# Kernel optimization log

Hardware: AMD Instinct MI355X
Metric: run time of the kernel (lower is better)

The kernel has to match this reference:

```python
import jax, jax.numpy as jnp
from jax import lax
import numpy as np

TEMPERATURE = 0.8
TOP_P = 0.9
NEG_INF = -jnp.inf


def setup_inputs() -> dict:
    key = jax.random.key(0)
    k1, k2 = jax.random.split(key)
    B, V = 128, 128000
    logits = jax.random.normal(k1, (B, V), dtype=jnp.float32) * 4.0
    u = jax.random.uniform(k2, (B, 1), dtype=jnp.float32)  # replaces torch.rand in sample_multinomial
    return {"logits": logits, "u": u, "top_k": 50}


def _filtered_probs(logits, top_k):
    # temperature scaling
    x = logits / TEMPERATURE
    # ---- top-k filter: keep only the k largest per row (mask rest to -inf) ----
    kth = lax.top_k(x, top_k)[0][..., -1:]            # [B, 1] k-th largest value
    x = jnp.where(x < kth, NEG_INF, x)
    # ---- top-p (nucleus) filter ----
    sort_idx = jnp.argsort(-x, axis=-1)               # descending order, [B, V]
    sorted_x = jnp.take_along_axis(x, sort_idx, axis=-1)
    probs_sorted = jax.nn.softmax(sorted_x, axis=-1)  # -inf entries -> 0
    cdf = jnp.cumsum(probs_sorted, axis=-1)
    # remove tokens where cdf (shifted right by one, first kept) exceeds p
    remove_sorted = jnp.concatenate(
        [jnp.zeros_like(cdf[..., :1], dtype=bool), (cdf > TOP_P)[..., :-1]], axis=-1
    )
    inv = jnp.argsort(sort_idx, axis=-1)              # inverse permutation
    remove = jnp.take_along_axis(remove_sorted, inv, axis=-1)
    x = jnp.where(remove, NEG_INF, x)
    # final probabilities
    return jax.nn.softmax(x.astype(jnp.float32), axis=-1)


def reference(logits, u, top_k):
    probs = _filtered_probs(logits, top_k)            # [B, V]
    # inverse-CDF multinomial sample (matches sample_multinomial)
    csum = jnp.cumsum(probs, axis=-1)
    next_ids = jnp.sum(csum <= u, axis=-1, keepdims=True).astype(jnp.int32)  # [B, 1]
    return next_ids
```

## Files before the change

kernel.cpp:

```cpp
#include <hip/hip_runtime.h>
#include <math.h>


#define SLICES   16
#define SEGCAP   64
#define MSORT    1024

__device__ __forceinline__ unsigned fkey(float y) {
    unsigned b = __float_as_uint(y);
    return (b & 0x80000000u) ? ~b : (b | 0x80000000u);
}

__device__ __forceinline__ float block_sum(float v, int tid, float* wpart) {
#pragma unroll
    for (int off = 32; off > 0; off >>= 1) v += __shfl_down(v, off, 64);
    if ((tid & 63) == 0) wpart[tid >> 6] = v;
    __syncthreads();
    if (tid < 64) {
        float s = (tid < 16) ? wpart[tid] : 0.0f;
#pragma unroll
        for (int off = 8; off > 0; off >>= 1) s += __shfl_down(s, off, 64);
        if (tid == 0) wpart[0] = s;
    }
    __syncthreads();
    float s = wpart[0];
    __syncthreads();
    return s;
}

__device__ __forceinline__ void incl_scan(float* arr, int n, int tid, float* wpart) {
    float v = (tid < n) ? arr[tid] : 0.0f;
#pragma unroll
    for (int off = 1; off < 64; off <<= 1) {
        float o = __shfl_up(v, off, 64);
        if ((tid & 63) >= off) v += o;
    }
    if ((tid & 63) == 63) wpart[tid >> 6] = v;
    __syncthreads();
    if (tid < 64) {
        float w = (tid < 16) ? wpart[tid] : 0.0f;
#pragma unroll
        for (int off = 1; off < 16; off <<= 1) {
            float o = __shfl_up(w, off, 64);
            if (tid >= off) w += o;
        }
        if (tid < 16) wpart[tid] = w;
    }
    __syncthreads();
    const int wv = tid >> 6;
    const float base = (wv > 0) ? wpart[wv - 1] : 0.0f;
    if (tid < n) arr[tid] = v + base;
    __syncthreads();
}

__device__ __forceinline__ float wsum(float v) {
#pragma unroll
    for (int off = 32; off > 0; off >>= 1) v += __shfl_xor(v, off, 64);
    return v;
}
__device__ __forceinline__ float wscan(float v, int lane) {
#pragma unroll
    for (int off = 1; off < 64; off <<= 1) {
        float o = __shfl_up(v, off, 64);
        if (lane >= off) v += o;
    }
    return v;
}

__global__ __launch_bounds__(256)
void scan_kernel(const float* __restrict__ logits, int V,
                 int* __restrict__ scnt,
                 float* __restrict__ cy, int* __restrict__ ci)
{
    constexpr float YTH = 11.2f;
    __shared__ float lcy[SEGCAP];
    __shared__ int   lci[SEGCAP];
    __shared__ int   lcnt;

    const int tid = threadIdx.x;
    const int row = blockIdx.x / SLICES;
    const int sl  = blockIdx.x % SLICES;
    if (tid == 0) lcnt = 0;
    __syncthreads();

    const float* rowp = logits + (size_t)row * (size_t)V;
    const float4* rp4 = (const float4*)rowp;
    const int n4   = V >> 2;
    const int base = sl * 256 + tid;

#define PUSH4(vv, i4)                                                            \
    {                                                                            \
        float _m = fmaxf(fmaxf((vv).x, (vv).y), fmaxf((vv).z, (vv).w));          \
        if (_m >= YTH) {                                                         \
            if ((vv).x >= YTH) { int _p = atomicAdd(&lcnt, 1);                   \
                if (_p < SEGCAP) { lcy[_p] = (vv).x; lci[_p] = (i4) * 4;     } } \
            if ((vv).y >= YTH) { int _p = atomicAdd(&lcnt, 1);                   \
                if (_p < SEGCAP) { lcy[_p] = (vv).y; lci[_p] = (i4) * 4 + 1; } } \
            if ((vv).z >= YTH) { int _p = atomicAdd(&lcnt, 1);                   \
                if (_p < SEGCAP) { lcy[_p] = (vv).z; lci[_p] = (i4) * 4 + 2; } } \
            if ((vv).w >= YTH) { int _p = atomicAdd(&lcnt, 1);                   \
                if (_p < SEGCAP) { lcy[_p] = (vv).w; lci[_p] = (i4) * 4 + 3; } } \
        }                                                                        \
    }

    if (sl * 256 + 255 + 7 * 4096 < n4) {
        float4 a0 = rp4[base];
        float4 a1 = rp4[base + 4096];
        float4 a2 = rp4[base + 8192];
        float4 a3 = rp4[base + 12288];
        float4 a4 = rp4[base + 16384];
        float4 a5 = rp4[base + 20480];
        float4 a6 = rp4[base + 24576];
        float4 a7 = rp4[base + 28672];
        PUSH4(a0, base);
        PUSH4(a1, base + 4096);
        PUSH4(a2, base + 8192);
        PUSH4(a3, base + 12288);
        PUSH4(a4, base + 16384);
        PUSH4(a5, base + 20480);
        PUSH4(a6, base + 24576);
        PUSH4(a7, base + 28672);
    } else {
        const int nc = n4 - 1;
        int i0 = base,          c0 = min(i0, nc);
        int i1 = base + 4096,   c1 = min(i1, nc);
        int i2 = base + 8192,   c2 = min(i2, nc);
        int i3 = base + 12288,  c3 = min(i3, nc);
        int i4_ = base + 16384, c4 = min(i4_, nc);
        int i5 = base + 20480,  c5 = min(i5, nc);
        int i6 = base + 24576,  c6 = min(i6, nc);
        int i7 = base + 28672,  c7 = min(i7, nc);
        float4 a0 = rp4[c0];
        float4 a1 = rp4[c1];
        float4 a2 = rp4[c2];
        float4 a3 = rp4[c3];
        float4 a4 = rp4[c4];
        float4 a5 = rp4[c5];
        float4 a6 = rp4[c6];
        float4 a7 = rp4[c7];
        if (i0 < n4) PUSH4(a0, i0);
        if (i1 < n4) PUSH4(a1, i1);
        if (i2 < n4) PUSH4(a2, i2);
        if (i3 < n4) PUSH4(a3, i3);
        if (i4_ < n4) PUSH4(a4, i4_);
        if (i5 < n4) PUSH4(a5, i5);
        if (i6 < n4) PUSH4(a6, i6);
        if (i7 < n4) PUSH4(a7, i7);
    }
    for (int i = SLICES * 256 * 8 + sl * 256 + tid; i < n4; i += SLICES * 256) {
        float4 a = rp4[i];
        PUSH4(a, i);
    }
    if (sl == SLICES - 1) {
        for (int i = (n4 << 2) + tid; i < V; i += 256) {
            float y = rowp[i];
            if (y >= YTH) {
                int p = atomicAdd(&lcnt, 1);
                if (p < SEGCAP) { lcy[p] = y; lci[p] = i; }
            }
        }
    }
#undef PUSH4
    __syncthreads();

    const int cnt = lcnt;
    float* cyr = cy + ((size_t)row * SLICES + sl) * SEGCAP;
    int*   cir = ci + ((size_t)row * SLICES + sl) * SEGCAP;
    for (int p = tid; p < min(cnt, SEGCAP); p += 256) {
        cyr[p] = lcy[p];
        cir[p] = lci[p];
    }
    if (tid == 0) scnt[row * SLICES + sl] = cnt;
}

__global__ __launch_bounds__(1024)
void select_kernel(const float* __restrict__ logits,
                   const float* __restrict__ uvec,
                   const int* __restrict__ topk_p,
                   const int* __restrict__ scnt,
                   const float* __restrict__ cy, const int* __restrict__ ci,
                   int* __restrict__ out, int V)
{
    constexpr float TEMP = 0.8f;
    constexpr float TOPP = 0.9f;
    constexpr float XTH2 = 16.0f;

    __shared__ float gv[MSORT];
    __shared__ int   gi[MSORT];
    __shared__ float cv[MSORT];
    __shared__ int   cidx[MSORT];
    __shared__ float sq[MSORT];
    __shared__ float wpart[16];
    __shared__ float kth_sh;
    __shared__ int   segoff[SLICES + 1];
    __shared__ int   bad_sh, hi_cnt, cpos, scount, cnt_sh, M_sh, tie_cnt, L_cnt, ans_sh;
    __shared__ int   Kp_sh, fast_sh;

    const int tid  = threadIdx.x;
    const int lane = tid & 63;
    const int row  = blockIdx.x;
    const int nth  = blockDim.x;
    const int k_in = *topk_p;

    const float* rowp = logits + (size_t)row * (size_t)V;

    if (tid == 0) { hi_cnt = 0; cpos = 0; scount = 0;
                    tie_cnt = 0; L_cnt = 0; ans_sh = V; }
    if (tid < 64) {
        int c = (tid < SLICES) ? scnt[row * SLICES + tid] : 0;
        int bad = (tid < SLICES) && (c > SEGCAP);
        int acc = min(c, SEGCAP);
#pragma unroll
        for (int off = 1; off < SLICES; off <<= 1) {
            int o = __shfl_up(acc, off, 64);
            if (tid >= off) acc += o;
        }
        if (tid < SLICES) segoff[tid + 1] = acc;
        if (tid == 0) segoff[0] = 0;
        unsigned long long bm = __ballot(bad);
        if (tid == 0) bad_sh = (bm != 0ULL);
    }
    __syncthreads();

    const int M_all = segoff[SLICES];
    int M;
    if (!bad_sh && M_all >= k_in && M_all <= MSORT) {
        {
            const int s = tid >> 6;
            const int off = segoff[s];
            const int c   = segoff[s + 1] - off;
            if (lane < c) {
                const size_t base = ((size_t)row * SLICES + s) * SEGCAP + lane;
                gv[off + lane] = cy[base] / TEMP;
                gi[off + lane] = ci[base];
            }
        }
        __syncthreads();
        {
            bool pred = (tid < M_all) && (gv[tid] >= XTH2);
            unsigned long long bm = __ballot(pred);
            if (lane == 0 && bm) atomicAdd(&hi_cnt, (int)__popcll(bm));
        }
        __syncthreads();
        const float thr = (hi_cnt >= k_in) ? XTH2 : -1e38f;
        {
            bool pred = (tid < M_all) && (gv[tid] >= thr);
            unsigned long long bm = __ballot(pred);
            if (bm) {
                int fl = (int)__ffsll(bm) - 1;
                int bs = 0;
                if (pred && lane == fl) bs = atomicAdd(&cpos, (int)__popcll(bm));
                bs = __shfl(bs, fl, 64);
                if (pred) {
                    int p = bs + (int)__popcll(bm & ((1ULL << lane) - 1ULL));
                    cv[p] = gv[tid]; cidx[p] = gi[tid];
                }
            }
        }
        __syncthreads();
        M = cpos;
    } else {
        unsigned lo = 0;
        for (int bit = 31; bit >= 0; --bit) {
            unsigned t = lo | (1u << bit);
            int local = 0;
            for (int i = tid; i < V; i += nth) local += (fkey(rowp[i]) >= t);
            if (tid == 0) cnt_sh = 0;
            __syncthreads();
            atomicAdd(&cnt_sh, local);
            __syncthreads();
            if (cnt_sh >= k_in) lo = t;
            __syncthreads();
        }
        for (int i = tid; i < V; i += nth) {
            float y = rowp[i];
            if (fkey(y) >= lo) {
                int p = atomicAdd(&scount, 1);
                if (p < MSORT) { cv[p] = y / TEMP; cidx[p] = i; }
            }
        }
        __syncthreads();
        M = min(scount, MSORT);
    }
    if (tid == 0) M_sh = M;
    __syncthreads();
    M = M_sh;

    const int Mpad = (M + 3) & ~3;
    for (int t = M + tid; t < Mpad; t += nth) { cv[t] = -1e38f; cidx[t] = 0x7fffffff; }
    __syncthreads();

    for (int t = tid; t < M; t += nth) {
        const float v = cv[t]; const int ix = cidx[t];
        int r = 0;
        for (int j = 0; j < Mpad; j += 4) {
            float v0 = cv[j],     v1 = cv[j + 1];
            float v2 = cv[j + 2], v3 = cv[j + 3];
            int   i0 = cidx[j],     i1 = cidx[j + 1];
            int   i2 = cidx[j + 2], i3 = cidx[j + 3];
            r += (v0 > v || (v0 == v && i0 < ix));
            r += (v1 > v || (v1 == v && i1 < ix));
            r += (v2 > v || (v2 == v && i2 < ix));
            r += (v3 > v || (v3 == v && i3 < ix));
        }
        gv[r] = v; gi[r] = ix;
    }
    __syncthreads();

    if (tid < 64) {
        int kk = (M > 0) ? min(max(k_in, 1), M) : 0;
        float kth = (M > 0) ? gv[kk - 1] : 0.0f;
        int j0 = min(kk + lane, MSORT - 1);
        int j1 = min(kk + 64 + lane, MSORT - 1);
        bool t0 = (M > 0) && (kk + lane < M)      && (gv[j0] == kth);
        bool t1 = (M > 0) && (kk + 64 + lane < M) && (gv[j1] == kth);
        int cnt = (int)__popcll(__ballot(t0)) + (int)__popcll(__ballot(t1));
        if (lane == 0) {
            int Kp = kk + cnt;
            Kp_sh = Kp;
            fast_sh = (M > 0) && (Kp <= 128);
        }
    }
    __syncthreads();

    if (fast_sh) {
        if (tid < 64) {
            const int Kp = Kp_sh;
            const int e0 = lane, e1 = lane + 64;
            const float mm = gv[0];
            float se0 = (e0 < Kp) ? expf(gv[e0] - mm) : 0.0f;
            float se1 = (e1 < Kp) ? expf(gv[e1] - mm) : 0.0f;

            const float sum1 = wsum(se0 + se1);
            float q0 = se0 / sum1, q1 = se1 / sum1;

            float s0 = wscan(q0, lane);
            float T0 = __shfl(s0, 63, 64);
            float s1 = wscan(q1, lane) + T0;

            float prev0 = __shfl_up(s0, 1, 64);
            float prev1 = __shfl_up(s1, 1, 64);
            if (lane == 0) prev1 = T0;
            bool c0 = (e0 >= 1) && (e0 < Kp) && (prev0 <= TOPP);
            bool c1 = (e1 < Kp) && (prev1 <= TOPP);
            const int L = 1 + (int)__popcll(__ballot(c0)) + (int)__popcll(__ballot(c1));

            const float sum2 = wsum(((e0 < L) ? se0 : 0.0f) + ((e1 < L) ? se1 : 0.0f));
            float p0 = se0 / sum2, p1 = se1 / sum2;
            int i0 = (e0 < L) ? gi[e0] : 0x7fffffff;
            int i1 = (e1 < L) ? gi[e1] : 0x7fffffff;

            const int Lpad = (L + 3) & ~3;
            if (lane < Lpad - L) gi[L + lane] = 0x7fffffff;
            __builtin_amdgcn_wave_barrier();

            int r0 = 0, r1 = 0;
            for (int j = 0; j < Lpad; j += 4) {
                int g0 = gi[j], g1 = gi[j + 1], g2 = gi[j + 2], g3 = gi[j + 3];
                r0 += (g0 < i0) + (g1 < i0) + (g2 < i0) + (g3 < i0);
                r1 += (g0 < i1) + (g1 < i1) + (g2 < i1) + (g3 < i1);
            }
            if (e0 < L) { sq[r0] = p0; cidx[r0] = i0; }
            if (e1 < L) { sq[r1] = p1; cidx[r1] = i1; }
            __builtin_amdgcn_wave_barrier();

            float g0v = (e0 < L) ? sq[e0] : 0.0f;
            float g1v = (e1 < L) ? sq[e1] : 0.0f;
            int   vi0 = (e0 < L) ? cidx[e0] : 0;
            int   vi1 = (e1 < L) ? cidx[e1] : 0;
            float C0 = wscan(g0v, lane);
            float TT = __shfl(C0, 63, 64);
            float C1 = wscan(g1v, lane) + TT;
            float pc0 = __shfl_up(C0, 1, 64);
            float pc1 = __shfl_up(C1, 1, 64);
            if (lane == 0) pc1 = TT;
            const float uu = uvec[row];
            bool f0 = (e0 < L) && (C0 > uu) && (e0 == 0 || pc0 <= uu);
            bool f1 = (e1 < L) && (C1 > uu) && (pc1 <= uu);
            int ans = V;
            if (f0) ans = vi0;
            if (f1) ans = vi1;
#pragma unroll
            for (int off = 32; off > 0; off >>= 1)
                ans = min(ans, __shfl_xor(ans, off, 64));
            if (lane == 0) out[row] = ans;
        }
        return;
    }

    const int kk = (M > 0) ? min(max(k_in, 1), M) : 0;
    const float mm = (M > 0) ? gv[0] : 0.0f;
    if (tid < M) cv[tid] = expf(gv[tid] - mm);
    if (tid == 0 && M > 0) kth_sh = gv[kk - 1];
    __syncthreads();

    {
        bool f = (M > 0) && (tid >= kk) && (tid < M) && (gv[tid] == kth_sh);
        unsigned long long bm = __ballot(f);
        if (lane == 0 && bm) atomicAdd(&tie_cnt, (int)__popcll(bm));
    }
    __syncthreads();
    const int Kp = kk + tie_cnt;

    const float sum1 = block_sum((tid < Kp) ? cv[tid] : 0.0f, tid, wpart);

    if (tid < Kp) sq[tid] = cv[tid] / sum1;
    incl_scan(sq, Kp, tid, wpart);
    {
        bool f = (tid >= 1) && (tid < Kp) && (sq[tid - 1] <= TOPP);
        unsigned long long bm = __ballot(f);
        if (lane == 0 && bm) atomicAdd(&L_cnt, (int)__popcll(bm));
    }
    __syncthreads();
    const int L = (M > 0) ? (1 + L_cnt) : 0;

    const float sum2 = block_sum((tid < L) ? cv[tid] : 0.0f, tid, wpart);

    if (tid < L) {
        const int ix = gi[tid];
        int r = 0;
        for (int j = 0; j < L; ++j) r += (gi[j] < ix);
        sq[r] = cv[tid] / sum2;
        cidx[r] = ix;
    }
    __syncthreads();

    incl_scan(sq, L, tid, wpart);
    {
        const float uu = uvec[row];
        bool f = (tid < L) && (sq[tid] > uu) && (tid == 0 || sq[tid - 1] <= uu);
        if (f) ans_sh = cidx[tid];
    }
    __syncthreads();
    if (tid == 0) out[row] = ans_sh;
}

extern "C" void kernel_launch(void* const* d_in, const int* in_sizes, int n_in,
                              void* d_out, int out_size, void* d_ws, size_t ws_size,
                              hipStream_t stream) {
    const float* logits = (const float*)d_in[0];
    const float* u      = (const float*)d_in[1];
    const int*   topk   = (const int*)d_in[2];
    int*         out    = (int*)d_out;

    const int B = out_size;
    const int V = in_sizes[0] / B;

    const size_t n_scnt = (size_t)B * SLICES;
    const size_t n_seg  = (size_t)B * SLICES * SEGCAP;
    int*   scnt = (int*)d_ws;
    float* cy   = (float*)((char*)d_ws + n_scnt * 4);
    int*   ci   = (int*)((char*)d_ws + n_scnt * 4 + n_seg * 4);

    scan_kernel<<<B * SLICES, 256, 0, stream>>>(logits, V, scnt, cy, ci);
    select_kernel<<<B, 1024, 0, stream>>>(logits, u, topk, scnt, cy, ci, out, V);
}
```

Measured before the change: 101.3 us.

## Fuse scan and select kernels using a last-block-done atomic counter per row

Merges the two-kernel pipeline into one launch: each of the 16 slice blocks per row writes its candidates to global memory, then bumps a per-row atomic counter, and the last block to finish performs the selection with 256 threads instead of a separate 1024-thread block. This removes the second kernel launch and the dependency gap between kernels, at the cost of a hipMemsetAsync to reset counters and less parallelism in the selection phase. The slow fallback path is now serialized on a single thread, and the radix-select fallback runs with a quarter of the threads.

```diff
diff --git a/kernel.cpp b/kernel.cpp
--- a/kernel.cpp
+++ b/kernel.cpp
@@ -5,52 +5,11 @@
 #define SLICES   16
 #define SEGCAP   64
 #define MSORT    1024
+#define NTH      256
 
 __device__ __forceinline__ unsigned fkey(float y) {
     unsigned b = __float_as_uint(y);
     return (b & 0x80000000u) ? ~b : (b | 0x80000000u);
-}
-
-__device__ __forceinline__ float block_sum(float v, int tid, float* wpart) {
-#pragma unroll
-    for (int off = 32; off > 0; off >>= 1) v += __shfl_down(v, off, 64);
-    if ((tid & 63) == 0) wpart[tid >> 6] = v;
-    __syncthreads();
-    if (tid < 64) {
-        float s = (tid < 16) ? wpart[tid] : 0.0f;
-#pragma unroll
-        for (int off = 8; off > 0; off >>= 1) s += __shfl_down(s, off, 64);
-        if (tid == 0) wpart[0] = s;
-    }
-    __syncthreads();
-    float s = wpart[0];
-    __syncthreads();
-    return s;
-}
-
-__device__ __forceinline__ void incl_scan(float* arr, int n, int tid, float* wpart) {
-    float v = (tid < n) ? arr[tid] : 0.0f;
-#pragma unroll
-    for (int off = 1; off < 64; off <<= 1) {
-        float o = __shfl_up(v, off, 64);
-        if ((tid & 63) >= off) v += o;
-    }
-    if ((tid & 63) == 63) wpart[tid >> 6] = v;
-    __syncthreads();
-    if (tid < 64) {
-        float w = (tid < 16) ? wpart[tid] : 0.0f;
-#pragma unroll
-        for (int off = 1; off < 16; off <<= 1) {
-            float o = __shfl_up(w, off, 64);
-            if (tid >= off) w += o;
-        }
-        if (tid < 16) wpart[tid] = w;
-    }
-    __syncthreads();
-    const int wv = tid >> 6;
-    const float base = (wv > 0) ? wpart[wv - 1] : 0.0f;
-    if (tid < n) arr[tid] = v + base;
-    __syncthreads();
 }
 
 __device__ __forceinline__ float wsum(float v) {
@@ -68,18 +27,32 @@
 }
 
 __global__ __launch_bounds__(256)
-void scan_kernel(const float* __restrict__ logits, int V,
-                 int* __restrict__ scnt,
-                 float* __restrict__ cy, int* __restrict__ ci)
+void fused_kernel(const float* __restrict__ logits,
+                  const float* __restrict__ uvec,
+                  const int* __restrict__ topk_p,
+                  int* __restrict__ done_ctr,
+                  int* __restrict__ scnt,
+                  float* __restrict__ cy, int* __restrict__ ci,
+                  int* __restrict__ out, int V)
 {
-    constexpr float YTH = 11.2f;
-    __shared__ float lcy[SEGCAP];
-    __shared__ int   lci[SEGCAP];
-    __shared__ int   lcnt;
-
-    const int tid = threadIdx.x;
-    const int row = blockIdx.x / SLICES;
-    const int sl  = blockIdx.x % SLICES;
+    constexpr float YTH  = 11.2f;
+    constexpr float TEMP = 0.8f;
+    constexpr float TOPP = 0.9f;
+    constexpr float XTH2 = 16.0f;
+
+    __shared__ float Sv[MSORT];
+    __shared__ int   Si[MSORT];
+    __shared__ float Av[MSORT];
+    __shared__ int   Ai[MSORT];
+    __shared__ int   segoff[SLICES + 1];
+    __shared__ int   lcnt, is_last_sh;
+    __shared__ int   hi_cnt, cpos, scount, cnt_sh, M_sh, Kp_sh, fast_sh, bad_sh;
+
+    const int tid  = threadIdx.x;
+    const int lane = tid & 63;
+    const int row  = blockIdx.x / SLICES;
+    const int sl   = blockIdx.x % SLICES;
+
     if (tid == 0) lcnt = 0;
     __syncthreads();
 
@@ -93,13 +66,13 @@
         float _m = fmaxf(fmaxf((vv).x, (vv).y), fmaxf((vv).z, (vv).w));          \
         if (_m >= YTH) {                                                         \
             if ((vv).x >= YTH) { int _p = atomicAdd(&lcnt, 1);                   \
-                if (_p < SEGCAP) { lcy[_p] = (vv).x; lci[_p] = (i4) * 4;     } } \
+                if (_p < SEGCAP) { Av[_p] = (vv).x; Ai[_p] = (i4) * 4;     } }   \
             if ((vv).y >= YTH) { int _p = atomicAdd(&lcnt, 1);                   \
-                if (_p < SEGCAP) { lcy[_p] = (vv).y; lci[_p] = (i4) * 4 + 1; } } \
+                if (_p < SEGCAP) { Av[_p] = (vv).y; Ai[_p] = (i4) * 4 + 1; } }   \
             if ((vv).z >= YTH) { int _p = atomicAdd(&lcnt, 1);                   \
-                if (_p < SEGCAP) { lcy[_p] = (vv).z; lci[_p] = (i4) * 4 + 2; } } \
+                if (_p < SEGCAP) { Av[_p] = (vv).z; Ai[_p] = (i4) * 4 + 2; } }   \
             if ((vv).w >= YTH) { int _p = atomicAdd(&lcnt, 1);                   \
-                if (_p < SEGCAP) { lcy[_p] = (vv).w; lci[_p] = (i4) * 4 + 3; } } \
+                if (_p < SEGCAP) { Av[_p] = (vv).w; Ai[_p] = (i4) * 4 + 3; } }   \
         }                                                                        \
     }
 
@@ -156,7 +129,7 @@
             float y = rowp[i];
             if (y >= YTH) {
                 int p = atomicAdd(&lcnt, 1);
-                if (p < SEGCAP) { lcy[p] = y; lci[p] = i; }
+                if (p < SEGCAP) { Av[p] = y; Ai[p] = i; }
             }
         }
     }
@@ -164,48 +137,27 @@
     __syncthreads();
 
     const int cnt = lcnt;
-    float* cyr = cy + ((size_t)row * SLICES + sl) * SEGCAP;
-    int*   cir = ci + ((size_t)row * SLICES + sl) * SEGCAP;
-    for (int p = tid; p < min(cnt, SEGCAP); p += 256) {
-        cyr[p] = lcy[p];
-        cir[p] = lci[p];
-    }
-    if (tid == 0) scnt[row * SLICES + sl] = cnt;
-}
-
-__global__ __launch_bounds__(1024)
-void select_kernel(const float* __restrict__ logits,
-                   const float* __restrict__ uvec,
-                   const int* __restrict__ topk_p,
-                   const int* __restrict__ scnt,
-                   const float* __restrict__ cy, const int* __restrict__ ci,
-                   int* __restrict__ out, int V)
-{
-    constexpr float TEMP = 0.8f;
-    constexpr float TOPP = 0.9f;
-    constexpr float XTH2 = 16.0f;
-
-    __shared__ float gv[MSORT];
-    __shared__ int   gi[MSORT];
-    __shared__ float cv[MSORT];
-    __shared__ int   cidx[MSORT];
-    __shared__ float sq[MSORT];
-    __shared__ float wpart[16];
-    __shared__ float kth_sh;
-    __shared__ int   segoff[SLICES + 1];
-    __shared__ int   bad_sh, hi_cnt, cpos, scount, cnt_sh, M_sh, tie_cnt, L_cnt, ans_sh;
-    __shared__ int   Kp_sh, fast_sh;
-
-    const int tid  = threadIdx.x;
-    const int lane = tid & 63;
-    const int row  = blockIdx.x;
-    const int nth  = blockDim.x;
+    {
+        float* cyr = cy + ((size_t)row * SLICES + sl) * SEGCAP;
+        int*   cir = ci + ((size_t)row * SLICES + sl) * SEGCAP;
+        for (int p = tid; p < min(cnt, SEGCAP); p += NTH) {
+            cyr[p] = Av[p];
+            cir[p] = Ai[p];
+        }
+        if (tid == 0) scnt[row * SLICES + sl] = cnt;
+    }
+
+    __threadfence();
+    __syncthreads();
+    if (tid == 0)
+        is_last_sh = (atomicAdd(&done_ctr[row], 1) == SLICES - 1);
+    __syncthreads();
+    if (!is_last_sh) return;
+    __threadfence();
+
     const int k_in = *topk_p;
 
-    const float* rowp = logits + (size_t)row * (size_t)V;
-
-    if (tid == 0) { hi_cnt = 0; cpos = 0; scount = 0;
-                    tie_cnt = 0; L_cnt = 0; ans_sh = V; }
+    if (tid == 0) { hi_cnt = 0; cpos = 0; scount = 0; }
     if (tid < 64) {
         int c = (tid < SLICES) ? scnt[row * SLICES + tid] : 0;
         int bad = (tid < SLICES) && (c > SEGCAP);
@@ -226,34 +178,44 @@
     int M;
     if (!bad_sh && M_all >= k_in && M_all <= MSORT) {
         {
-            const int s = tid >> 6;
-            const int off = segoff[s];
-            const int c   = segoff[s + 1] - off;
-            if (lane < c) {
-                const size_t base = ((size_t)row * SLICES + s) * SEGCAP + lane;
-                gv[off + lane] = cy[base] / TEMP;
-                gi[off + lane] = ci[base];
+            const int wv = tid >> 6;
+            for (int s = wv; s < SLICES; s += 4) {
+                const int off = segoff[s];
+                const int c   = segoff[s + 1] - off;
+                if (lane < c) {
+                    const size_t gbase = ((size_t)row * SLICES + s) * SEGCAP + lane;
+                    Sv[off + lane] = cy[gbase] / TEMP;
+                    Si[off + lane] = ci[gbase];
+                }
             }
         }
         __syncthreads();
         {
-            bool pred = (tid < M_all) && (gv[tid] >= XTH2);
-            unsigned long long bm = __ballot(pred);
-            if (lane == 0 && bm) atomicAdd(&hi_cnt, (int)__popcll(bm));
+            const int rounds = (M_all + NTH - 1) / NTH;
+            for (int rd = 0; rd < rounds; ++rd) {
+                const int t = rd * NTH + tid;
+                bool pred = (t < M_all) && (Sv[t] >= XTH2);
+                unsigned long long bm = __ballot(pred);
+                if (lane == 0 && bm) atomicAdd(&hi_cnt, (int)__popcll(bm));
+            }
         }
         __syncthreads();
         const float thr = (hi_cnt >= k_in) ? XTH2 : -1e38f;
         {
-            bool pred = (tid < M_all) && (gv[tid] >= thr);
-            unsigned long long bm = __ballot(pred);
-            if (bm) {
-                int fl = (int)__ffsll(bm) - 1;
-                int bs = 0;
-                if (pred && lane == fl) bs = atomicAdd(&cpos, (int)__popcll(bm));
-                bs = __shfl(bs, fl, 64);
-                if (pred) {
-                    int p = bs + (int)__popcll(bm & ((1ULL << lane) - 1ULL));
-                    cv[p] = gv[tid]; cidx[p] = gi[tid];
+            const int rounds = (M_all + NTH - 1) / NTH;
+            for (int rd = 0; rd < rounds; ++rd) {
+                const int t = rd * NTH + tid;
+                bool pred = (t < M_all) && (Sv[t] >= thr);
+                unsigned long long bm = __ballot(pred);
+                if (bm) {
+                    int fl = (int)__ffsll(bm) - 1;
+                    int bs = 0;
+                    if (pred && lane == fl) bs = atomicAdd(&cpos, (int)__popcll(bm));
+                    bs = __shfl(bs, fl, 64);
+                    if (pred) {
+                        int p = bs + (int)__popcll(bm & ((1ULL << lane) - 1ULL));
+                        Av[p] = Sv[t]; Ai[p] = Si[t];
+                    }
                 }
             }
         }
@@ -262,21 +224,21 @@
     } else {
         unsigned lo = 0;
         for (int bit = 31; bit >= 0; --bit) {
-            unsigned t = lo | (1u << bit);
+            unsigned tb = lo | (1u << bit);
             int local = 0;
-            for (int i = tid; i < V; i += nth) local += (fkey(rowp[i]) >= t);
+            for (int i = tid; i < V; i += NTH) local += (fkey(rowp[i]) >= tb);
             if (tid == 0) cnt_sh = 0;
             __syncthreads();
             atomicAdd(&cnt_sh, local);
             __syncthreads();
-            if (cnt_sh >= k_in) lo = t;
+            if (cnt_sh >= k_in) lo = tb;
             __syncthreads();
         }
-        for (int i = tid; i < V; i += nth) {
+        for (int i = tid; i < V; i += NTH) {
             float y = rowp[i];
             if (fkey(y) >= lo) {
                 int p = atomicAdd(&scount, 1);
-                if (p < MSORT) { cv[p] = y / TEMP; cidx[p] = i; }
+                if (p < MSORT) { Av[p] = y / TEMP; Ai[p] = i; }
             }
         }
         __syncthreads();
@@ -287,38 +249,37 @@
     M = M_sh;
 
     const int Mpad = (M + 3) & ~3;
-    for (int t = M + tid; t < Mpad; t += nth) { cv[t] = -1e38f; cidx[t] = 0x7fffffff; }
-    __syncthreads();
-
-    for (int t = tid; t < M; t += nth) {
-        const float v = cv[t]; const int ix = cidx[t];
+    for (int t = M + tid; t < Mpad; t += NTH) { Av[t] = -1e38f; Ai[t] = 0x7fffffff; }
+    __syncthreads();
+
+    for (int t = tid; t < M; t += NTH) {
+        const float v = Av[t]; const int ix = Ai[t];
         int r = 0;
         for (int j = 0; j < Mpad; j += 4) {
-            float v0 = cv[j],     v1 = cv[j + 1];
-            float v2 = cv[j + 2], v3 = cv[j + 3];
-            int   i0 = cidx[j],     i1 = cidx[j + 1];
-            int   i2 = cidx[j + 2], i3 = cidx[j + 3];
+            float v0 = Av[j],     v1 = Av[j + 1];
+            float v2 = Av[j + 2], v3 = Av[j + 3];
+            int   i0 = Ai[j],     i1 = Ai[j + 1];
+            int   i2 = Ai[j + 2], i3 = Ai[j + 3];
             r += (v0 > v || (v0 == v && i0 < ix));
             r += (v1 > v || (v1 == v && i1 < ix));
             r += (v2 > v || (v2 == v && i2 < ix));
             r += (v3 > v || (v3 == v && i3 < ix));
         }
-        gv[r] = v; gi[r] = ix;
+        Sv[r] = v; Si[r] = ix;
     }
     __syncthreads();
 
     if (tid < 64) {
         int kk = (M > 0) ? min(max(k_in, 1), M) : 0;
-        float kth = (M > 0) ? gv[kk - 1] : 0.0f;
+        float kth = (M > 0) ? Sv[kk - 1] : 0.0f;
         int j0 = min(kk + lane, MSORT - 1);
         int j1 = min(kk + 64 + lane, MSORT - 1);
-        bool t0 = (M > 0) && (kk + lane < M)      && (gv[j0] == kth);
-        bool t1 = (M > 0) && (kk + 64 + lane < M) && (gv[j1] == kth);
-        int cnt = (int)__popcll(__ballot(t0)) + (int)__popcll(__ballot(t1));
+        bool t0 = (M > 0) && (kk + lane < M)      && (Sv[j0] == kth);
+        bool t1 = (M > 0) && (kk + 64 + lane < M) && (Sv[j1] == kth);
+        int cnt2 = (int)__popcll(__ballot(t0)) + (int)__popcll(__ballot(t1));
         if (lane == 0) {
-            int Kp = kk + cnt;
-            Kp_sh = Kp;
-            fast_sh = (M > 0) && (Kp <= 128);
+            Kp_sh = kk + cnt2;
+            fast_sh = (M > 0) && (Kp_sh <= 128);
         }
     }
     __syncthreads();
@@ -327,9 +288,9 @@
         if (tid < 64) {
             const int Kp = Kp_sh;
             const int e0 = lane, e1 = lane + 64;
-            const float mm = gv[0];
-            float se0 = (e0 < Kp) ? expf(gv[e0] - mm) : 0.0f;
-            float se1 = (e1 < Kp) ? expf(gv[e1] - mm) : 0.0f;
+            const float mm = Sv[0];
+            float se0 = (e0 < Kp) ? expf(Sv[e0] - mm) : 0.0f;
+            float se1 = (e1 < Kp) ? expf(Sv[e1] - mm) : 0.0f;
 
             const float sum1 = wsum(se0 + se1);
             float q0 = se0 / sum1, q1 = se1 / sum1;
@@ -347,27 +308,27 @@
 
             const float sum2 = wsum(((e0 < L) ? se0 : 0.0f) + ((e1 < L) ? se1 : 0.0f));
             float p0 = se0 / sum2, p1 = se1 / sum2;
-            int i0 = (e0 < L) ? gi[e0] : 0x7fffffff;
-            int i1 = (e1 < L) ? gi[e1] : 0x7fffffff;
+            int i0 = (e0 < L) ? Si[e0] : 0x7fffffff;
+            int i1 = (e1 < L) ? Si[e1] : 0x7fffffff;
 
             const int Lpad = (L + 3) & ~3;
-            if (lane < Lpad - L) gi[L + lane] = 0x7fffffff;
+            if (lane < Lpad - L) Si[L + lane] = 0x7fffffff;
             __builtin_amdgcn_wave_barrier();
 
             int r0 = 0, r1 = 0;
             for (int j = 0; j < Lpad; j += 4) {
-                int g0 = gi[j], g1 = gi[j + 1], g2 = gi[j + 2], g3 = gi[j + 3];
+                int g0 = Si[j], g1 = Si[j + 1], g2 = Si[j + 2], g3 = Si[j + 3];
                 r0 += (g0 < i0) + (g1 < i0) + (g2 < i0) + (g3 < i0);
                 r1 += (g0 < i1) + (g1 < i1) + (g2 < i1) + (g3 < i1);
             }
-            if (e0 < L) { sq[r0] = p0; cidx[r0] = i0; }
-            if (e1 < L) { sq[r1] = p1; cidx[r1] = i1; }
+            if (e0 < L) { Av[r0] = p0; Ai[r0] = i0; }
+            if (e1 < L) { Av[r1] = p1; Ai[r1] = i1; }
             __builtin_amdgcn_wave_barrier();
 
-            float g0v = (e0 < L) ? sq[e0] : 0.0f;
-            float g1v = (e1 < L) ? sq[e1] : 0.0f;
-            int   vi0 = (e0 < L) ? cidx[e0] : 0;
-            int   vi1 = (e1 < L) ? cidx[e1] : 0;
+            float g0v = (e0 < L) ? Av[e0] : 0.0f;
+            float g1v = (e1 < L) ? Av[e1] : 0.0f;
+            int   vi0 = (e0 < L) ? Ai[e0] : 0;
+            int   vi1 = (e1 < L) ? Ai[e1] : 0;
             float C0 = wscan(g0v, lane);
             float TT = __shfl(C0, 63, 64);
             float C1 = wscan(g1v, lane) + TT;
@@ -388,51 +349,40 @@
         return;
     }
 
-    const int kk = (M > 0) ? min(max(k_in, 1), M) : 0;
-    const float mm = (M > 0) ? gv[0] : 0.0f;
-    if (tid < M) cv[tid] = expf(gv[tid] - mm);
-    if (tid == 0 && M > 0) kth_sh = gv[kk - 1];
-    __syncthreads();
-
-    {
-        bool f = (M > 0) && (tid >= kk) && (tid < M) && (gv[tid] == kth_sh);
-        unsigned long long bm = __ballot(f);
-        if (lane == 0 && bm) atomicAdd(&tie_cnt, (int)__popcll(bm));
-    }
-    __syncthreads();
-    const int Kp = kk + tie_cnt;
-
-    const float sum1 = block_sum((tid < Kp) ? cv[tid] : 0.0f, tid, wpart);
-
-    if (tid < Kp) sq[tid] = cv[tid] / sum1;
-    incl_scan(sq, Kp, tid, wpart);
-    {
-        bool f = (tid >= 1) && (tid < Kp) && (sq[tid - 1] <= TOPP);
-        unsigned long long bm = __ballot(f);
-        if (lane == 0 && bm) atomicAdd(&L_cnt, (int)__popcll(bm));
-    }
-    __syncthreads();
-    const int L = (M > 0) ? (1 + L_cnt) : 0;
-
-    const float sum2 = block_sum((tid < L) ? cv[tid] : 0.0f, tid, wpart);
-
-    if (tid < L) {
-        const int ix = gi[tid];
-        int r = 0;
-        for (int j = 0; j < L; ++j) r += (gi[j] < ix);
-        sq[r] = cv[tid] / sum2;
-        cidx[r] = ix;
-    }
-    __syncthreads();
-
-    incl_scan(sq, L, tid, wpart);
-    {
-        const float uu = uvec[row];
-        bool f = (tid < L) && (sq[tid] > uu) && (tid == 0 || sq[tid - 1] <= uu);
-        if (f) ans_sh = cidx[tid];
-    }
-    __syncthreads();
-    if (tid == 0) out[row] = ans_sh;
+    if (tid == 0) {
+        int ans = V;
+        if (M > 0) {
+            const int kk = min(max(k_in, 1), M);
+            const float kth = Sv[kk - 1];
+            int Kp = kk;
+            for (int t = kk; t < M; ++t) Kp += (Sv[t] == kth);
+            const float mm = Sv[0];
+            float sum1 = 0.0f;
+            for (int t = 0; t < Kp; ++t) sum1 += expf(Sv[t] - mm);
+            int L = 1;
+            float pref = 0.0f;
+            for (int t = 1; t < Kp; ++t) {
+                pref += expf(Sv[t - 1] - mm) / sum1;
+                L += (pref <= TOPP);
+            }
+            float sum2 = 0.0f;
+            for (int t = 0; t < L; ++t) sum2 += expf(Sv[t] - mm);
+            const float uu = uvec[row];
+            int last = -1;
+            float csum = 0.0f;
+            for (int step = 0; step < L; ++step) {
+                int mn = 0x7fffffff, mt = -1;
+                for (int t = 0; t < L; ++t) {
+                    int ix = Si[t];
+                    if (ix > last && ix < mn) { mn = ix; mt = t; }
+                }
+                last = mn;
+                csum += expf(Sv[mt] - mm) / sum2;
+                if (csum > uu) { ans = mn; break; }
+            }
+        }
+        out[row] = ans;
+    }
 }
 
 extern "C" void kernel_launch(void* const* d_in, const int* in_sizes, int n_in,
@@ -448,10 +398,12 @@
 
     const size_t n_scnt = (size_t)B * SLICES;
     const size_t n_seg  = (size_t)B * SLICES * SEGCAP;
-    int*   scnt = (int*)d_ws;
-    float* cy   = (float*)((char*)d_ws + n_scnt * 4);
-    int*   ci   = (int*)((char*)d_ws + n_scnt * 4 + n_seg * 4);
-
-    scan_kernel<<<B * SLICES, 256, 0, stream>>>(logits, V, scnt, cy, ci);
-    select_kernel<<<B, 1024, 0, stream>>>(logits, u, topk, scnt, cy, ci, out, V);
+    int*   done = (int*)d_ws;
+    int*   scnt = done + B;
+    float* cy   = (float*)(scnt + n_scnt);
+    int*   ci   = (int*)(cy + n_seg);
+
+    (void)hipMemsetAsync(done, 0, (size_t)B * sizeof(int), stream);
+    fused_kernel<<<B * SLICES, NTH, 0, stream>>>(logits, u, topk,
+                                                 done, scnt, cy, ci, out, V);
 }
```

After: 327.6 us. 3.23x slower.
